# Optimization experiments

Measured on AMD Instinct MI355X. Metric: run time of the kernel, lower is better.

## Reference

```python
import jax, jax.numpy as jnp
import numpy as np

NUM_BLOCKS = 2
RES_LAYERS = 10
RC, DC, SC, EC, OC, GC = 32, 32, 1024, 512, 256, 5
RF = NUM_BLOCKS * (2 ** RES_LAYERS - 1)  # receptive/residual field = 2046


def _conv(x, w, dil, pad_left):
    # x: (N, C, L), w: (O, I, K). Causal: left pad only (equivalent to
    # torch padding=d followed by slicing off the last d samples).
    return jax.lax.conv_general_dilated(
        x, w, window_strides=(1,), padding=[(pad_left, 0)],
        rhs_dilation=(dil,), dimension_numbers=('NCH', 'OIH', 'NCH'))


def setup_inputs() -> dict:
    key = jax.random.key(0)
    ks = jax.random.split(key, 13)
    B, L = 2, 8192
    nl = NUM_BLOCKS * RES_LAYERS
    s = lambda k, shape, sc: (jax.random.normal(k, shape, jnp.float32) * sc)
    return {
        'inputs': s(ks[0], (B, 256, L), 1.0),
        'conditioning': s(ks[1], (B, GC), 1.0),
        'input_w': s(ks[2], (RC, 256, 1), 0.06),
        'filter_w': s(ks[3], (nl, DC, RC, 2), 0.12),
        'gate_w': s(ks[4], (nl, DC, RC, 2), 0.12),
        'res_w': s(ks[5], (nl, RC, DC, 1), 0.17),
        'split_w': s(ks[6], (nl, SC, DC, 1), 0.17),
        'gcf_w': s(ks[7], (nl, 1, GC), 0.3),
        'gcs_w': s(ks[8], (nl, 1, GC), 0.3),
        'f1_w': s(ks[9], (EC, SC, 1), 0.03),
        'f1_b': jnp.zeros((EC,), jnp.float32),
        'f2_w': s(ks[10], (OC, EC, 1), 0.04),
        'f2_b': jnp.zeros((OC,), jnp.float32),
    }


def reference(inputs, conditioning, input_w, filter_w, gate_w, res_w,
              split_w, gcf_w, gcs_w, f1_w, f1_b, f2_w, f2_b):
    L = inputs.shape[2]
    tgt = L - RF  # target_length
    res = _conv(inputs, input_w, 1, 0)  # (B, RC, L)
    final = jnp.zeros((inputs.shape[0], SC, tgt), inputs.dtype)
    for b in range(NUM_BLOCKS):
        for l in range(RES_LAYERS):
            i = b * RES_LAYERS + l
            d = 2 ** l
            f = _conv(res, filter_w[i], d, d)  # causal dilated, length L
            g = _conv(res, gate_w[i], d, d)
            # global conditioning: Linear(GC,1) -> per-batch scalar, broadcast
            gc_f = (conditioning @ gcf_w[i].T)[:, None, :]  # (B,1,1)
            gc_g = (conditioning @ gcs_w[i].T)[:, None, :]
            out = jnp.tanh(f + gc_f) * jax.nn.sigmoid(g + gc_g)
            res = _conv(out, res_w[i], 1, 0) + res
            final = final + _conv(out, split_w[i], 1, 0)[:, :, -tgt:]
    x = jax.nn.relu(final)
    x = _conv(x, f1_w, 1, 0) + f1_b[None, :, None]
    x = jax.nn.relu(x)
    x = _conv(x, f2_w, 1, 0) + f2_b[None, :, None]
    n, c, ln = x.shape
    return jnp.transpose(x, (0, 2, 1)).reshape(n * ln, c)
```

## Files before the change

### kernel.cpp

```cpp
#include <hip/hip_runtime.h>
#include <hip/hip_bf16.h>
#include <cstddef>

#define Bc   2
#define Lc   8192
#define TGT  6146
#define NL   20
#define RCc  32
#define DCc  32
#define SCc  1024
#define ECc  512
#define OCc  256
#define KTOT (NL * DCc)
#define TTILES 49
#define T64   97

typedef __attribute__((ext_vector_type(4))) float f32x4;
typedef __attribute__((ext_vector_type(8))) short bf16x8;
typedef __attribute__((ext_vector_type(4))) int i32x4;
typedef __attribute__((ext_vector_type(2))) int i32x2;

typedef __attribute__((address_space(1))) void* as1v;
typedef __attribute__((address_space(3))) void* as3v;

__device__ inline bf16x8 cvt8(const float4* p) {
    float4 a = p[0], b = p[1];
    union { bf16x8 v; __hip_bfloat16 h[8]; } u;
    u.h[0] = __float2bfloat16(a.x); u.h[1] = __float2bfloat16(a.y);
    u.h[2] = __float2bfloat16(a.z); u.h[3] = __float2bfloat16(a.w);
    u.h[4] = __float2bfloat16(b.x); u.h[5] = __float2bfloat16(b.y);
    u.h[6] = __float2bfloat16(b.z); u.h[7] = __float2bfloat16(b.w);
    return u.v;
}

__global__ __launch_bounds__(256) void prep_kernel(
    const float* __restrict__ x,
    const float* __restrict__ iw,
    float* __restrict__ res_out,
    const float* __restrict__ split_w,
    const float* __restrict__ f1_w,
    const float* __restrict__ f2_w,
    const float* __restrict__ filt,
    const float* __restrict__ gate,
    const float* __restrict__ resw,
    __hip_bfloat16* __restrict__ Wp1,
    __hip_bfloat16* __restrict__ Wp2,
    __hip_bfloat16* __restrict__ Wp3,
    __hip_bfloat16* __restrict__ wfgp,
    __hip_bfloat16* __restrict__ wrp,
    int npack)
{
    __shared__ float ws[32][256];
    __shared__ float xs[64][64];
    int tid = threadIdx.x;

    if ((int)blockIdx.x < npack) {
        int idx = blockIdx.x * 256 + tid;
        const int N1 = SCc * KTOT, N2 = ECc * SCc, N3 = OCc * ECc, N4 = NL * 64 * 64;
        if (idx < N1) {
            int m = idx / KTOT, k = idx % KTOT;
            int i = k >> 5, c = k & 31;
            Wp1[idx] = __float2bfloat16(split_w[((size_t)i * SCc + m) * DCc + c]);
            return;
        }
        idx -= N1;
        if (idx < N2) { Wp2[idx] = __float2bfloat16(f1_w[idx]); return; }
        idx -= N2;
        if (idx < N3) { Wp3[idx] = __float2bfloat16(f2_w[idx]); return; }
        idx -= N3;
        if (idx < N4) {
            int li = idx / 4096, r = idx % 4096;
            int m = r >> 6, k = r & 63;
            int tap = k >> 5, ic = k & 31;
            float v = (m < 32) ? filt[(size_t)li * 2048 + (m * 32 + ic) * 2 + tap]
                               : gate[(size_t)li * 2048 + ((m - 32) * 32 + ic) * 2 + tap];
            int slot = (k >> 3) ^ (m & 7);
            wfgp[((size_t)li * 64 + m) * 64 + slot * 8 + (k & 7)] = __float2bfloat16(v);
            if (r < 2048) {
                int m2 = r >> 6;
                float v2 = (k < 32) ? resw[(size_t)li * 1024 + m2 * 32 + k] : 0.f;
                wrp[((size_t)li * 32 + m2) * 64 + slot * 8 + (k & 7)] = __float2bfloat16(v2);
            }
        }
        return;
    }

    int bid = blockIdx.x - npack;
    int b   = bid >> 7;
    int t0  = (bid & 127) * 64;

    for (int idx = tid; idx < 32 * 256; idx += 256)
        ws[idx >> 8][idx & 255] = iw[idx];

    int tl = tid & 63, qq = tid >> 6, oc0 = qq * 8;
    float acc[8] = {};

    for (int icc = 0; icc < 4; ++icc) {
        __syncthreads();
        for (int idx = tid; idx < 64 * 64; idx += 256) {
            int icl = idx >> 6, tll = idx & 63;
            xs[icl][tll] = x[((size_t)b * 256 + icc * 64 + icl) * Lc + t0 + tll];
        }
        __syncthreads();
        for (int icl = 0; icl < 64; icl += 4) {
            float x0 = xs[icl][tl], x1 = xs[icl + 1][tl];
            float x2 = xs[icl + 2][tl], x3 = xs[icl + 3][tl];
#pragma unroll
            for (int j = 0; j < 8; ++j) {
                const float4 w4 = *(const float4*)&ws[oc0 + j][icc * 64 + icl];
                acc[j] += w4.x * x0 + w4.y * x1 + w4.z * x2 + w4.w * x3;
            }
        }
    }
#pragma unroll
    for (int j = 0; j < 8; ++j)
        res_out[((size_t)b * 32 + oc0 + j) * Lc + t0 + tl] = acc[j];
}

__global__ __launch_bounds__(512) void layer_group5(
    const float* __restrict__ res_in,
    float* __restrict__ res_out,
    __hip_bfloat16* __restrict__ outsT,
    const __hip_bfloat16* __restrict__ wfgp,
    const __hip_bfloat16* __restrict__ wrp,
    const float* __restrict__ cond,
    const float* __restrict__ gcf_w,
    const float* __restrict__ gcs_w,
    int l0)
{
    constexpr int W = 96, H = 32, NT = 6;
    __shared__ __align__(16) float resL[W * 36];
    __shared__ __align__(16) unsigned short OsL[W * 40];
    __shared__ __align__(16) i32x4 Wf[2][64 * 8];
    __shared__ __align__(16) i32x4 Wrs[2][32 * 8];

    int tid  = threadIdx.x;
    int b    = blockIdx.y;
    int t0   = blockIdx.x * 64;
    int lane = tid & 63, wid = tid >> 6;
    int r15  = lane & 15, q = lane >> 4;

    const float* rb = res_in + (size_t)b * 32 * Lc;
    for (int idx = tid; idx < W * 32; idx += 512) {
        int ch = idx / W, tl = idx % W;
        int tg = t0 - H + tl;
        resL[tl * 36 + ch] = (tg >= 0) ? rb[(size_t)ch * Lc + tg] : 0.f;
    }

    auto issueW = [&](int bufi, int li2) {
        const __hip_bfloat16* wfg = wfgp + (size_t)li2 * 4096;
        const __hip_bfloat16* wrl = wrp  + (size_t)li2 * 2048;
        __builtin_amdgcn_global_load_lds(
            (as1v)(void*)((const i32x4*)wfg + wid * 64 + lane),
            (as3v)(void*)&Wf[bufi][wid * 64], 16, 0, 0);
        if (wid < 4)
            __builtin_amdgcn_global_load_lds(
                (as1v)(void*)((const i32x4*)wrl + wid * 64 + lane),
                (as3v)(void*)&Wrs[bufi][wid * 64], 16, 0, 0);
    };
    issueW(0, l0);

#pragma unroll
    for (int i = 0; i < 5; ++i) {
        const int cur = i & 1;
        int li = l0 + i;
        int d  = 1 << i;

        float gf = 0.f, gg = 0.f;
#pragma unroll
        for (int c = 0; c < 5; ++c) {
            gf += gcf_w[li * 5 + c] * cond[b * 5 + c];
            gg += gcs_w[li * 5 + c] * cond[b * 5 + c];
        }
        __syncthreads();
        if (i + 1 < 5) issueW(cur ^ 1, li + 1);

        const bf16x8* Wv = (const bf16x8*)Wf[cur];
        for (int tt = wid; tt < NT; tt += 8) {
            int ct0 = tt * 16;
            int srow0 = ct0 + r15 - d; if (srow0 < 0) srow0 = 0;
            int srow1 = ct0 + r15;
            bf16x8 a0 = cvt8((const float4*)&resL[srow0 * 36 + q * 8]);
            bf16x8 a1 = cvt8((const float4*)&resL[srow1 * 36 + q * 8]);
            int sg0 = q ^ (r15 & 7), sg1 = (4 + q) ^ (r15 & 7);
            f32x4 acc[4] = {};
#pragma unroll
            for (int fj = 0; fj < 4; ++fj)
                acc[fj] = __builtin_amdgcn_mfma_f32_16x16x32_bf16(
                    a0, Wv[(fj * 16 + r15) * 8 + sg0], acc[fj], 0, 0, 0);
#pragma unroll
            for (int fj = 0; fj < 4; ++fj)
                acc[fj] = __builtin_amdgcn_mfma_f32_16x16x32_bf16(
                    a1, Wv[(fj * 16 + r15) * 8 + sg1], acc[fj], 0, 0, 0);
#pragma unroll
            for (int fj = 0; fj < 2; ++fj) {
#pragma unroll
                for (int r = 0; r < 4; ++r) {
                    float F = acc[fj][r] + gf;
                    float G = acc[fj + 2][r] + gg;
                    float th  = 1.f - 2.f / (__expf(2.f * F) + 1.f);
                    float sgm = 1.f / (1.f + __expf(-G));
                    float o   = th * sgm;
                    int col = ct0 + q * 4 + r;
                    int ch  = fj * 16 + r15;
                    __hip_bfloat16 ob = __float2bfloat16(o);
                    OsL[col * 40 + ch] = *(unsigned short*)&ob;
                }
            }
        }
        __syncthreads();

        {
            int row = tid >> 3, chunk = tid & 7;
            int tg = t0 + row;
            if (tg >= Lc - TGT) {
                i32x2 v = *(const i32x2*)&OsL[(H + row) * 40 + chunk * 4];
                *(i32x2*)(outsT + ((size_t)(b * TGT + tg - (Lc - TGT))) * KTOT
                          + li * 32 + chunk * 4) = v;
            }
        }

        const bf16x8* Rv = (const bf16x8*)Wrs[cur];
        const bf16x8* Ov = (const bf16x8*)OsL;
        for (int tt = wid; tt < NT; tt += 8) {
            int ct0 = tt * 16;
            bf16x8 ao = Ov[(ct0 + r15) * 5 + q];
            int sg = q ^ (r15 & 7);
            f32x4 racc[2] = {};
#pragma unroll
            for (int fj = 0; fj < 2; ++fj)
                racc[fj] = __builtin_amdgcn_mfma_f32_16x16x32_bf16(
                    ao, Rv[(fj * 16 + r15) * 8 + sg], racc[fj], 0, 0, 0);
#pragma unroll
            for (int fj = 0; fj < 2; ++fj)
#pragma unroll
                for (int r = 0; r < 4; ++r) {
                    int col = ct0 + q * 4 + r;
                    int ch  = fj * 16 + r15;
                    if (t0 + col - H >= 0)
                        resL[col * 36 + ch] += racc[fj][r];
                }
        }
    }
    __syncthreads();

    {
        int ch = tid >> 4, t4 = (tid & 15) * 4;
        float v[4];
#pragma unroll
        for (int j = 0; j < 4; ++j) v[j] = resL[(H + t4 + j) * 36 + ch];
        float* ro = res_out + ((size_t)(b * 32) + ch) * Lc + t0 + t4;
        *(float4*)ro = make_float4(v[0], v[1], v[2], v[3]);
    }
}

template <bool LASTHALF>
__global__ __launch_bounds__(512) void layer_groupS(
    const float* __restrict__ res_in,
    float* __restrict__ res_out,
    __hip_bfloat16* __restrict__ outsT,
    const __hip_bfloat16* __restrict__ wfgp,
    const __hip_bfloat16* __restrict__ wrp,
    const float* __restrict__ cond,
    const float* __restrict__ gcf_w,
    const float* __restrict__ gcs_w,
    int l0)
{
    constexpr int W = 96, H = 32, NT = 6, S = 32;
    __shared__ __align__(16) float resL[W * 36];
    __shared__ __align__(16) unsigned short OsL[W * 40];
    __shared__ __align__(16) i32x4 Wf[2][64 * 8];
    __shared__ __align__(16) i32x4 Wrs[2][32 * 8];

    int tid  = threadIdx.x;
    int b    = blockIdx.y;
    int r    = blockIdx.x & 31;
    int c0   = (blockIdx.x >> 5) * 64;
    int lane = tid & 63, wid = tid >> 6;
    int r15  = lane & 15, q = lane >> 4;

    const float* rb = res_in + (size_t)b * 32 * Lc;
    for (int idx = tid; idx < W * 32; idx += 512) {
        int ch = idx / W, col = idx % W;
        int cj = c0 + col - H;
        resL[col * 36 + ch] = (cj >= 0) ? rb[(size_t)ch * Lc + r + S * cj] : 0.f;
    }

    auto issueW = [&](int bufi, int li2) {
        const __hip_bfloat16* wfg = wfgp + (size_t)li2 * 4096;
        const __hip_bfloat16* wrl = wrp  + (size_t)li2 * 2048;
        __builtin_amdgcn_global_load_lds(
            (as1v)(void*)((const i32x4*)wfg + wid * 64 + lane),
            (as3v)(void*)&Wf[bufi][wid * 64], 16, 0, 0);
        if (wid < 4)
            __builtin_amdgcn_global_load_lds(
                (as1v)(void*)((const i32x4*)wrl + wid * 64 + lane),
                (as3v)(void*)&Wrs[bufi][wid * 64], 16, 0, 0);
    };
    issueW(0, l0);

#pragma unroll
    for (int i = 0; i < 5; ++i) {
        const int cur = i & 1;
        int li = l0 + i;
        int dc = 1 << i;

        float gf = 0.f, gg = 0.f;
#pragma unroll
        for (int c = 0; c < 5; ++c) {
            gf += gcf_w[li * 5 + c] * cond[b * 5 + c];
            gg += gcs_w[li * 5 + c] * cond[b * 5 + c];
        }
        __syncthreads();
        if (i + 1 < 5) issueW(cur ^ 1, li + 1);

        const bf16x8* Wv = (const bf16x8*)Wf[cur];
        for (int tt = wid; tt < NT; tt += 8) {
            int ct0 = tt * 16;
            int srow0 = ct0 + r15 - dc; if (srow0 < 0) srow0 = 0;
            int srow1 = ct0 + r15;
            bf16x8 a0 = cvt8((const float4*)&resL[srow0 * 36 + q * 8]);
            bf16x8 a1 = cvt8((const float4*)&resL[srow1 * 36 + q * 8]);
            int sg0 = q ^ (r15 & 7), sg1 = (4 + q) ^ (r15 & 7);
            f32x4 acc[4] = {};
#pragma unroll
            for (int fj = 0; fj < 4; ++fj)
                acc[fj] = __builtin_amdgcn_mfma_f32_16x16x32_bf16(
                    a0, Wv[(fj * 16 + r15) * 8 + sg0], acc[fj], 0, 0, 0);
#pragma unroll
            for (int fj = 0; fj < 4; ++fj)
                acc[fj] = __builtin_amdgcn_mfma_f32_16x16x32_bf16(
                    a1, Wv[(fj * 16 + r15) * 8 + sg1], acc[fj], 0, 0, 0);
#pragma unroll
            for (int fj = 0; fj < 2; ++fj) {
#pragma unroll
                for (int rr = 0; rr < 4; ++rr) {
                    float F = acc[fj][rr] + gf;
                    float G = acc[fj + 2][rr] + gg;
                    float th  = 1.f - 2.f / (__expf(2.f * F) + 1.f);
                    float sgm = 1.f / (1.f + __expf(-G));
                    float o   = th * sgm;
                    int col = ct0 + q * 4 + rr;
                    int ch  = fj * 16 + r15;
                    __hip_bfloat16 ob = __float2bfloat16(o);
                    OsL[col * 40 + ch] = *(unsigned short*)&ob;
                }
            }
        }
        __syncthreads();

        {
            int row = tid >> 3, chunk = tid & 7;
            int t = r + S * (c0 + row);
            if (t >= Lc - TGT) {
                i32x2 v = *(const i32x2*)&OsL[(H + row) * 40 + chunk * 4];
                *(i32x2*)(outsT + ((size_t)(b * TGT + t - (Lc - TGT))) * KTOT
                          + li * 32 + chunk * 4) = v;
            }
        }

        if (!(LASTHALF && i == 4)) {
            const bf16x8* Rv = (const bf16x8*)Wrs[cur];
            const bf16x8* Ov = (const bf16x8*)OsL;
            for (int tt = wid; tt < NT; tt += 8) {
                int ct0 = tt * 16;
                bf16x8 ao = Ov[(ct0 + r15) * 5 + q];
                int sg = q ^ (r15 & 7);
                f32x4 racc[2] = {};
#pragma unroll
                for (int fj = 0; fj < 2; ++fj)
                    racc[fj] = __builtin_amdgcn_mfma_f32_16x16x32_bf16(
                        ao, Rv[(fj * 16 + r15) * 8 + sg], racc[fj], 0, 0, 0);
#pragma unroll
                for (int fj = 0; fj < 2; ++fj)
#pragma unroll
                    for (int rr = 0; rr < 4; ++rr) {
                        int col = ct0 + q * 4 + rr;
                        int ch  = fj * 16 + r15;
                        if (c0 + col - H >= 0)
                            resL[col * 36 + ch] += racc[fj][rr];
                    }
            }
        }
    }

    if (!LASTHALF) {
        __syncthreads();
        int ch = tid >> 4, t4 = (tid & 15) * 4;
#pragma unroll
        for (int j = 0; j < 4; ++j) {
            int t = r + S * (c0 + t4 + j);
            res_out[((size_t)(b * 32) + ch) * Lc + t] = resL[(H + t4 + j) * 36 + ch];
        }
    }
}

template <bool RELU_OUT, int NKT>
__global__ __launch_bounds__(256) void gemm_mfma64(
    const __hip_bfloat16* __restrict__ X,
    const __hip_bfloat16* __restrict__ W,
    const float* __restrict__ bias,
    __hip_bfloat16* __restrict__ Y,
    int M, int MB)
{
    constexpr int K = NKT * 64;
    __shared__ __align__(16) char smem[49152];
    i32x4* Xs0 = (i32x4*)smem;
    i32x4* Ws0 = (i32x4*)(smem + 16384);
    i32x4* Xs1 = (i32x4*)(smem + 24576);
    i32x4* Ws1 = (i32x4*)(smem + 40960);

    int nwg  = gridDim.x;
    int orig = blockIdx.x;
    int q8 = nwg >> 3, r8 = nwg & 7;
    int xcd = orig & 7, loc = orig >> 3;
    int wgid = (xcd < r8 ? xcd * (q8 + 1) : r8 * (q8 + 1) + (xcd - r8) * q8) + loc;
    int mi  = wgid % MB;
    int byy = wgid / MB;
    int b   = byy / TTILES;
    int t0  = (byy % TTILES) * 128;
    int m0  = mi * 64;

    int tid = threadIdx.x;
    int lane = tid & 63, wid = tid >> 6;
    int r15 = lane & 15, q = lane >> 4;

    int subrow = lane >> 3;
    int g      = (lane & 7) ^ subrow;
    const __hip_bfloat16* xp[4];
    const __hip_bfloat16* wp[2];
#pragma unroll
    for (int i = 0; i < 4; ++i) {
        int r = wid * 32 + i * 8 + subrow;
        int xrow = t0 + r; if (xrow > TGT - 1) xrow = TGT - 1;
        xp[i] = X + ((size_t)(b * TGT + xrow)) * K + g * 8;
    }
#pragma unroll
    for (int i = 0; i < 2; ++i) {
        int r = wid * 16 + i * 8 + subrow;
        wp[i] = W + ((size_t)(m0 + r)) * K + g * 8;
    }

    f32x4 acc[2][4] = {};

#define STAGE(XB, WB)                                                          \
    {                                                                          \
        _Pragma("unroll")                                                      \
        for (int i = 0; i < 4; ++i) {                                          \
            __builtin_amdgcn_global_load_lds((as1v)(void*)xp[i],               \
                (as3v)(void*)&XB[(wid * 4 + i) * 64], 16, 0, 0);               \
            xp[i] += 64;                                                       \
        }                                                                      \
        _Pragma("unroll")                                                      \
        for (int i = 0; i < 2; ++i) {                                          \
            __builtin_amdgcn_global_load_lds((as1v)(void*)wp[i],               \
                (as3v)(void*)&WB[(wid * 2 + i) * 64], 16, 0, 0);               \
            wp[i] += 64;                                                       \
        }                                                                      \
    }

    auto compute = [&](const i32x4* Xb, const i32x4* Wb) {
        const bf16x8* Xv = (const bf16x8*)Xb;
        const bf16x8* Wv = (const bf16x8*)Wb;
#pragma unroll
        for (int kk = 0; kk < 2; ++kk) {
            int sg = (kk * 4 + q) ^ (r15 & 7);
            bf16x8 af[2], bw[4];
#pragma unroll
            for (int ft = 0; ft < 2; ++ft)
                af[ft] = Xv[(wid * 32 + ft * 16 + r15) * 8 + sg];
#pragma unroll
            for (int fj = 0; fj < 4; ++fj)
                bw[fj] = Wv[(fj * 16 + r15) * 8 + sg];
#pragma unroll
            for (int ft = 0; ft < 2; ++ft)
#pragma unroll
                for (int fj = 0; fj < 4; ++fj)
                    acc[ft][fj] = __builtin_amdgcn_mfma_f32_16x16x32_bf16(
                        af[ft], bw[fj], acc[ft][fj], 0, 0, 0);
        }
    };

    STAGE(Xs0, Ws0);

#pragma unroll
    for (int kt2 = 0; kt2 < NKT; kt2 += 2) {
        STAGE(Xs1, Ws1);
        asm volatile("s_waitcnt vmcnt(6)" ::: "memory");
        __builtin_amdgcn_s_barrier();
        __builtin_amdgcn_sched_barrier(0);
        __builtin_amdgcn_s_setprio(1);
        compute(Xs0, Ws0);
        __builtin_amdgcn_s_setprio(0);
        __builtin_amdgcn_sched_barrier(0);
        __builtin_amdgcn_s_barrier();

        if (kt2 + 2 < NKT) {
            STAGE(Xs0, Ws0);
            asm volatile("s_waitcnt vmcnt(6)" ::: "memory");
        } else {
            asm volatile("s_waitcnt vmcnt(0)" ::: "memory");
        }
        __builtin_amdgcn_s_barrier();
        __builtin_amdgcn_sched_barrier(0);
        __builtin_amdgcn_s_setprio(1);
        compute(Xs1, Ws1);
        __builtin_amdgcn_s_setprio(0);
        __builtin_amdgcn_sched_barrier(0);
        __builtin_amdgcn_s_barrier();
    }
#undef STAGE

    __hip_bfloat16* Eb = (__hip_bfloat16*)smem;
#pragma unroll
    for (int ft = 0; ft < 2; ++ft) {
#pragma unroll
        for (int r = 0; r < 4; ++r) {
            int tl = wid * 32 + ft * 16 + q * 4 + r;
#pragma unroll
            for (int fj = 0; fj < 4; ++fj) {
                int ml = fj * 16 + r15;
                float v = acc[ft][fj][r];
                if (bias) v += bias[m0 + ml];
                if (RELU_OUT) v = fmaxf(v, 0.f);
                Eb[tl * 72 + ml] = __float2bfloat16(v);
            }
        }
    }
    __syncthreads();
    {
        int row = tid >> 1, half = tid & 1;
        int t = t0 + row;
        if (t < TGT) {
            __hip_bfloat16* dst = Y + ((size_t)(b * TGT + t)) * M + m0 + half * 32;
            const __hip_bfloat16* src = Eb + row * 72 + half * 32;
#pragma unroll
            for (int k = 0; k < 4; ++k)
                ((i32x4*)dst)[k] = ((const i32x4*)src)[k];
        }
    }
}

__global__ __launch_bounds__(512) void gemm_fused23(
    const __hip_bfloat16* __restrict__ X,
    const __hip_bfloat16* __restrict__ W2,
    const float* __restrict__ b1,
    const __hip_bfloat16* __restrict__ W3,
    const float* __restrict__ b2,
    float* __restrict__ Y)
{
    __shared__ __align__(16) char smem[153600];
    i32x4* Xs[2] = { (i32x4*)smem, (i32x4*)(smem + 8192) };
    i32x4* Ws[2] = { (i32x4*)(smem + 16384), (i32x4*)(smem + 81920) };
    __hip_bfloat16* Hs = (__hip_bfloat16*)(smem + 16384);
    i32x4* W3s[2] = { (i32x4*)(smem + 88064), (i32x4*)(smem + 120832) };

    int nwg  = gridDim.x;
    int orig = blockIdx.x;
    int q8 = nwg >> 3, r8 = nwg & 7;
    int xcd = orig & 7, loc = orig >> 3;
    int wgid = (xcd < r8 ? xcd * (q8 + 1) : r8 * (q8 + 1) + (xcd - r8) * q8) + loc;
    int b  = wgid / T64;
    int t0 = (wgid % T64) * 64;

    int tid = threadIdx.x;
    int lane = tid & 63, wid = tid >> 6;
    int r15 = lane & 15, q = lane >> 4;
    int subrow = lane >> 3;
    int g      = (lane & 7) ^ subrow;

    int xr = wid * 8 + subrow;
    int xrow = t0 + xr; if (xrow > TGT - 1) xrow = TGT - 1;
    const __hip_bfloat16* xp = X + ((size_t)(b * TGT + xrow)) * SCc + g * 8;
    const __hip_bfloat16* wp[8];
#pragma unroll
    for (int i = 0; i < 8; ++i)
        wp[i] = W2 + ((size_t)((wid * 8 + i) * 8 + subrow)) * SCc + g * 8;

    f32x4 acc[4][4] = {};

#define STAGEA(bi)                                                             \
    {                                                                          \
        __builtin_amdgcn_global_load_lds((as1v)(void*)xp,                      \
            (as3v)(void*)&Xs[bi][wid * 64], 16, 0, 0);                         \
        xp += 64;                                                              \
        _Pragma("unroll")                                                      \
        for (int i = 0; i < 8; ++i) {                                          \
            __builtin_amdgcn_global_load_lds((as1v)(void*)wp[i],               \
                (as3v)(void*)&Ws[bi][(wid * 8 + i) * 64], 16, 0, 0);           \
            wp[i] += 64;                                                       \
        }                                                                      \
    }

    auto computeA = [&](const i32x4* Xb, const i32x4* Wb) {
        const bf16x8* Xv = (const bf16x8*)Xb;
        const bf16x8* Wv = (const bf16x8*)Wb;
#pragma unroll
        for (int kk = 0; kk < 2; ++kk) {
            int sg = (kk * 4 + q) ^ (r15 & 7);
            bf16x8 af[4], bw[4];
#pragma unroll
            for (int ft = 0; ft < 4; ++ft)
                af[ft] = Xv[(ft * 16 + r15) * 8 + sg];
#pragma unroll
            for (int fj = 0; fj < 4; ++fj)
                bw[fj] = Wv[(wid * 64 + fj * 16 + r15) * 8 + sg];
#pragma unroll
            for (int ft = 0; ft < 4; ++ft)
#pragma unroll
                for (int fj = 0; fj < 4; ++fj)
                    acc[ft][fj] = __builtin_amdgcn_mfma_f32_16x16x32_bf16(
                        af[ft], bw[fj], acc[ft][fj], 0, 0, 0);
        }
    };

    STAGEA(0);
#pragma unroll
    for (int kt = 0; kt < 16; ++kt) {
        const int cur = kt & 1;
        if (kt + 1 < 16) {
            STAGEA(cur ^ 1);
            asm volatile("s_waitcnt vmcnt(9)" ::: "memory");
        } else {
            asm volatile("s_waitcnt vmcnt(0)" ::: "memory");
        }
        __builtin_amdgcn_s_barrier();
        __builtin_amdgcn_sched_barrier(0);
        __builtin_amdgcn_s_setprio(1);
        computeA(Xs[cur], Ws[cur]);
        __builtin_amdgcn_s_setprio(0);
        __builtin_amdgcn_sched_barrier(0);
        __builtin_amdgcn_s_barrier();
    }
#undef STAGEA

#pragma unroll
    for (int ft = 0; ft < 4; ++ft) {
#pragma unroll
        for (int r = 0; r < 4; ++r) {
            int tl = ft * 16 + q * 4 + r;
#pragma unroll
            for (int fj = 0; fj < 4; ++fj) {
                int m = wid * 64 + fj * 16 + r15;
                float v = acc[ft][fj][r] + b1[m];
                v = fmaxf(v, 0.f);
                Hs[tl * 520 + m] = __float2bfloat16(v);
            }
        }
    }

    const __hip_bfloat16* w3p[4];
#pragma unroll
    for (int i = 0; i < 4; ++i)
        w3p[i] = W3 + ((size_t)((wid * 4 + i) * 8 + subrow)) * ECc + g * 8;

#define STAGEB(bi)                                                             \
    {                                                                          \
        _Pragma("unroll")                                                      \
        for (int i = 0; i < 4; ++i) {                                          \
            __builtin_amdgcn_global_load_lds((as1v)(void*)w3p[i],              \
                (as3v)(void*)&W3s[bi][(wid * 4 + i) * 64], 16, 0, 0);          \
            w3p[i] += 64;                                                      \
        }                                                                      \
    }

    STAGEB(0);
    __syncthreads();

    f32x4 accB[4][2] = {};

#pragma unroll
    for (int kt = 0; kt < 8; ++kt) {
        const int cur = kt & 1;
        if (kt + 1 < 8) {
            STAGEB(cur ^ 1);
            asm volatile("s_waitcnt vmcnt(4)" ::: "memory");
        } else {
            asm volatile("s_waitcnt vmcnt(0)" ::: "memory");
        }
        __builtin_amdgcn_s_barrier();
        __builtin_amdgcn_sched_barrier(0);
        __builtin_amdgcn_s_setprio(1);
        {
            const bf16x8* Wv = (const bf16x8*)W3s[cur];
#pragma unroll
            for (int kk = 0; kk < 2; ++kk) {
                int gk = kt * 8 + kk * 4 + q;
                int sg = (kk * 4 + q) ^ (r15 & 7);
                bf16x8 af[4], bw[2];
#pragma unroll
                for (int ft = 0; ft < 4; ++ft)
                    af[ft] = *(const bf16x8*)&Hs[(ft * 16 + r15) * 520 + gk * 8];
#pragma unroll
                for (int fj = 0; fj < 2; ++fj)
                    bw[fj] = Wv[(wid * 32 + fj * 16 + r15) * 8 + sg];
#pragma unroll
                for (int ft = 0; ft < 4; ++ft)
#pragma unroll
                    for (int fj = 0; fj < 2; ++fj)
                        accB[ft][fj] = __builtin_amdgcn_mfma_f32_16x16x32_bf16(
                            af[ft], bw[fj], accB[ft][fj], 0, 0, 0);
            }
        }
        __builtin_amdgcn_s_setprio(0);
        __builtin_amdgcn_sched_barrier(0);
        __builtin_amdgcn_s_barrier();
    }
#undef STAGEB

#pragma unroll
    for (int ft = 0; ft < 4; ++ft) {
#pragma unroll
        for (int r = 0; r < 4; ++r) {
            int t = t0 + ft * 16 + q * 4 + r;
            if (t < TGT) {
                size_t rowoff = ((size_t)(b * TGT + t)) * OCc;
#pragma unroll
                for (int fj = 0; fj < 2; ++fj) {
                    int m = wid * 32 + fj * 16 + r15;
                    Y[rowoff + m] = accB[ft][fj][r] + b2[m];
                }
            }
        }
    }
}

extern "C" void kernel_launch(void* const* d_in, const int* in_sizes, int n_in,
                              void* d_out, int out_size, void* d_ws, size_t ws_size,
                              hipStream_t stream)
{
    const float* inputs   = (const float*)d_in[0];
    const float* cond     = (const float*)d_in[1];
    const float* input_w  = (const float*)d_in[2];
    const float* filter_w = (const float*)d_in[3];
    const float* gate_w   = (const float*)d_in[4];
    const float* res_w    = (const float*)d_in[5];
    const float* split_w  = (const float*)d_in[6];
    const float* gcf_w    = (const float*)d_in[7];
    const float* gcs_w    = (const float*)d_in[8];
    const float* f1_w     = (const float*)d_in[9];
    const float* f1_b     = (const float*)d_in[10];
    const float* f2_w     = (const float*)d_in[11];
    const float* f2_b     = (const float*)d_in[12];
    float* out = (float*)d_out;

    char* wsb = (char*)d_ws;
    const size_t RES_B   = (size_t)Bc * RCc * Lc * 4;
    const size_t OUTS_B  = (size_t)Bc * TGT * KTOT * 2;
    const size_t FIN_B   = (size_t)Bc * TGT * SCc * 2;
    const size_t W1_B    = (size_t)SCc * KTOT * 2;
    const size_t W2_B    = (size_t)ECc * SCc * 2;
    const size_t W3_B    = (size_t)OCc * ECc * 2;
    const size_t WFG_B   = (size_t)NL * 64 * 64 * 2;
    const size_t WR_B    = (size_t)NL * 32 * 64 * 2;

    float* res0              = (float*)wsb;                   size_t off = RES_B;
    float* res1              = (float*)(wsb + off);           off += RES_B;
    __hip_bfloat16* outsT    = (__hip_bfloat16*)(wsb + off);  off += OUTS_B;
    __hip_bfloat16* finalT   = (__hip_bfloat16*)(wsb + off);  off += FIN_B;
    __hip_bfloat16* Wp1      = (__hip_bfloat16*)(wsb + off);  off += W1_B;
    __hip_bfloat16* Wp2      = (__hip_bfloat16*)(wsb + off);  off += W2_B;
    __hip_bfloat16* Wp3      = (__hip_bfloat16*)(wsb + off);  off += W3_B;
    __hip_bfloat16* wfgp     = (__hip_bfloat16*)(wsb + off);  off += WFG_B;
    __hip_bfloat16* wrp      = (__hip_bfloat16*)(wsb + off);  off += WR_B;

    {
        const int NTOT = SCc * KTOT + ECc * SCc + OCc * ECc + NL * 64 * 64;
        const int npack = (NTOT + 255) / 256;
        prep_kernel<<<npack + Bc * 128, 256, 0, stream>>>(
            inputs, input_w, res0,
            split_w, f1_w, f2_w, filter_w, gate_w, res_w,
            Wp1, Wp2, Wp3, wfgp, wrp, npack);
    }

    float* rin = res0;
    float* rout = res1;
    const dim3 lgrid(Lc / 64, Bc);
    const dim3 sgrid(128, Bc);

    layer_group5<<<lgrid, 512, 0, stream>>>(
        rin, rout, outsT, wfgp, wrp, cond, gcf_w, gcs_w, 0);
    { float* t = rin; rin = rout; rout = t; }
    layer_groupS<false><<<sgrid, 512, 0, stream>>>(
        rin, rout, outsT, wfgp, wrp, cond, gcf_w, gcs_w, 5);
    { float* t = rin; rin = rout; rout = t; }
    layer_group5<<<lgrid, 512, 0, stream>>>(
        rin, rout, outsT, wfgp, wrp, cond, gcf_w, gcs_w, 10);
    { float* t = rin; rin = rout; rout = t; }
    layer_groupS<true><<<sgrid, 512, 0, stream>>>(
        rin, rout, outsT, wfgp, wrp, cond, gcf_w, gcs_w, 15);

    gemm_mfma64<true, 10><<<(SCc / 64) * Bc * TTILES, 256, 0, stream>>>(
        outsT, Wp1, nullptr, finalT, SCc, SCc / 64);

    gemm_fused23<<<Bc * T64, 512, 0, stream>>>(
        finalT, Wp2, f1_b, Wp3, f2_b, out);
}
```

Before: 163.1 us.

## Double-buffer residual tile in LDS, drop mid-layer barrier, skip unneeded early tiles

The residual tile in LDS is split into two ping-pong buffers (resA/resB). Each wave now owns one 16-column tile and does the gated activation, the outsT store and the residual MFMA update without the barrier that used to sit between them, leaving one __syncthreads per layer. The third layer-group launch also starts at tile 15 and skips early time tiles. Causality means those tiles cannot reach the target window or later layers. The cost is more LDS per block, which may lower occupancy, and a reliance on intra-wave ordering of LDS writes and reads.

Measured after the change: 156.3 us, median of 3. 1.04x faster.

```diff
diff --git a/kernel.cpp b/kernel.cpp
--- a/kernel.cpp
+++ b/kernel.cpp
@@ -126,17 +126,18 @@
     const float* __restrict__ cond,
     const float* __restrict__ gcf_w,
     const float* __restrict__ gcs_w,
-    int l0)
+    int l0, int t0off)
 {
     constexpr int W = 96, H = 32, NT = 6;
-    __shared__ __align__(16) float resL[W * 36];
+    __shared__ __align__(16) float resA[W * 36];
+    __shared__ __align__(16) float resB[W * 36];
     __shared__ __align__(16) unsigned short OsL[W * 40];
     __shared__ __align__(16) i32x4 Wf[2][64 * 8];
     __shared__ __align__(16) i32x4 Wrs[2][32 * 8];
 
     int tid  = threadIdx.x;
     int b    = blockIdx.y;
-    int t0   = blockIdx.x * 64;
+    int t0   = (t0off + blockIdx.x) * 64;
     int lane = tid & 63, wid = tid >> 6;
     int r15  = lane & 15, q = lane >> 4;
 
@@ -144,7 +145,7 @@
     for (int idx = tid; idx < W * 32; idx += 512) {
         int ch = idx / W, tl = idx % W;
         int tg = t0 - H + tl;
-        resL[tl * 36 + ch] = (tg >= 0) ? rb[(size_t)ch * Lc + tg] : 0.f;
+        resA[tl * 36 + ch] = (tg >= 0) ? rb[(size_t)ch * Lc + tg] : 0.f;
     }
 
     auto issueW = [&](int bufi, int li2) {
@@ -163,6 +164,8 @@
 #pragma unroll
     for (int i = 0; i < 5; ++i) {
         const int cur = i & 1;
+        const float* rc = cur ? resB : resA;
+        float*       rn = cur ? resA : resB;
         int li = l0 + i;
         int d  = 1 << i;
 
@@ -175,13 +178,13 @@
         __syncthreads();
         if (i + 1 < 5) issueW(cur ^ 1, li + 1);
 
-        const bf16x8* Wv = (const bf16x8*)Wf[cur];
-        for (int tt = wid; tt < NT; tt += 8) {
-            int ct0 = tt * 16;
+        if (wid < NT) {
+            int ct0 = wid * 16;
+            const bf16x8* Wv = (const bf16x8*)Wf[cur];
             int srow0 = ct0 + r15 - d; if (srow0 < 0) srow0 = 0;
             int srow1 = ct0 + r15;
-            bf16x8 a0 = cvt8((const float4*)&resL[srow0 * 36 + q * 8]);
-            bf16x8 a1 = cvt8((const float4*)&resL[srow1 * 36 + q * 8]);
+            bf16x8 a0 = cvt8((const float4*)&rc[srow0 * 36 + q * 8]);
+            bf16x8 a1 = cvt8((const float4*)&rc[srow1 * 36 + q * 8]);
             int sg0 = q ^ (r15 & 7), sg1 = (4 + q) ^ (r15 & 7);
             f32x4 acc[4] = {};
 #pragma unroll
@@ -207,23 +210,20 @@
                     OsL[col * 40 + ch] = *(unsigned short*)&ob;
                 }
             }
-        }
-        __syncthreads();
-
-        {
-            int row = tid >> 3, chunk = tid & 7;
-            int tg = t0 + row;
-            if (tg >= Lc - TGT) {
-                i32x2 v = *(const i32x2*)&OsL[(H + row) * 40 + chunk * 4];
-                *(i32x2*)(outsT + ((size_t)(b * TGT + tg - (Lc - TGT))) * KTOT
-                          + li * 32 + chunk * 4) = v;
-            }
-        }
-
-        const bf16x8* Rv = (const bf16x8*)Wrs[cur];
-        const bf16x8* Ov = (const bf16x8*)OsL;
-        for (int tt = wid; tt < NT; tt += 8) {
-            int ct0 = tt * 16;
+
+            {
+                int col = ct0 + (lane >> 2), chunk = lane & 3;
+                if (col >= H) {
+                    int t = t0 + col - H;
+                    if (t >= Lc - TGT)
+                        *(i32x4*)(outsT + ((size_t)(b * TGT + t - (Lc - TGT))) * KTOT
+                                  + li * 32 + chunk * 8) =
+                            *(const i32x4*)&OsL[col * 40 + chunk * 8];
+                }
+            }
+
+            const bf16x8* Rv = (const bf16x8*)Wrs[cur];
+            const bf16x8* Ov = (const bf16x8*)OsL;
             bf16x8 ao = Ov[(ct0 + r15) * 5 + q];
             int sg = q ^ (r15 & 7);
             f32x4 racc[2] = {};
@@ -237,8 +237,8 @@
                 for (int r = 0; r < 4; ++r) {
                     int col = ct0 + q * 4 + r;
                     int ch  = fj * 16 + r15;
-                    if (t0 + col - H >= 0)
-                        resL[col * 36 + ch] += racc[fj][r];
+                    float base = rc[col * 36 + ch];
+                    rn[col * 36 + ch] = (t0 + col - H >= 0) ? base + racc[fj][r] : base;
                 }
         }
     }
@@ -248,7 +248,7 @@
         int ch = tid >> 4, t4 = (tid & 15) * 4;
         float v[4];
 #pragma unroll
-        for (int j = 0; j < 4; ++j) v[j] = resL[(H + t4 + j) * 36 + ch];
+        for (int j = 0; j < 4; ++j) v[j] = resB[(H + t4 + j) * 36 + ch];
         float* ro = res_out + ((size_t)(b * 32) + ch) * Lc + t0 + t4;
         *(float4*)ro = make_float4(v[0], v[1], v[2], v[3]);
     }
@@ -267,7 +267,8 @@
     int l0)
 {
     constexpr int W = 96, H = 32, NT = 6, S = 32;
-    __shared__ __align__(16) float resL[W * 36];
+    __shared__ __align__(16) float resA[W * 36];
+    __shared__ __align__(16) float resB[W * 36];
     __shared__ __align__(16) unsigned short OsL[W * 40];
     __shared__ __align__(16) i32x4 Wf[2][64 * 8];
     __shared__ __align__(16) i32x4 Wrs[2][32 * 8];
@@ -283,7 +284,7 @@
     for (int idx = tid; idx < W * 32; idx += 512) {
         int ch = idx / W, col = idx % W;
         int cj = c0 + col - H;
-        resL[col * 36 + ch] = (cj >= 0) ? rb[(size_t)ch * Lc + r + S * cj] : 0.f;
+        resA[col * 36 + ch] = (cj >= 0) ? rb[(size_t)ch * Lc + r + S * cj] : 0.f;
     }
 
     auto issueW = [&](int bufi, int li2) {
@@ -302,6 +303,8 @@
 #pragma unroll
     for (int i = 0; i < 5; ++i) {
         const int cur = i & 1;
+        const float* rc = cur ? resB : resA;
+        float*       rn = cur ? resA : resB;
         int li = l0 + i;
         int dc = 1 << i;
 
@@ -314,13 +317,13 @@
         __syncthreads();
         if (i + 1 < 5) issueW(cur ^ 1, li + 1);
 
-        const bf16x8* Wv = (const bf16x8*)Wf[cur];
-        for (int tt = wid; tt < NT; tt += 8) {
-            int ct0 = tt * 16;
+        if (wid < NT) {
+            int ct0 = wid * 16;
+            const bf16x8* Wv = (const bf16x8*)Wf[cur];
             int srow0 = ct0 + r15 - dc; if (srow0 < 0) srow0 = 0;
             int srow1 = ct0 + r15;
-            bf16x8 a0 = cvt8((const float4*)&resL[srow0 * 36 + q * 8]);
-            bf16x8 a1 = cvt8((const float4*)&resL[srow1 * 36 + q * 8]);
+            bf16x8 a0 = cvt8((const float4*)&rc[srow0 * 36 + q * 8]);
+            bf16x8 a1 = cvt8((const float4*)&rc[srow1 * 36 + q * 8]);
             int sg0 = q ^ (r15 & 7), sg1 = (4 + q) ^ (r15 & 7);
             f32x4 acc[4] = {};
 #pragma unroll
@@ -346,24 +349,21 @@
                     OsL[col * 40 + ch] = *(unsigned short*)&ob;
                 }
             }
-        }
-        __syncthreads();
-
-        {
-            int row = tid >> 3, chunk = tid & 7;
-            int t = r + S * (c0 + row);
-            if (t >= Lc - TGT) {
-                i32x2 v = *(const i32x2*)&OsL[(H + row) * 40 + chunk * 4];
-                *(i32x2*)(outsT + ((size_t)(b * TGT + t - (Lc - TGT))) * KTOT
-                          + li * 32 + chunk * 4) = v;
-            }
-        }
-
-        if (!(LASTHALF && i == 4)) {
-            const bf16x8* Rv = (const bf16x8*)Wrs[cur];
-            const bf16x8* Ov = (const bf16x8*)OsL;
-            for (int tt = wid; tt < NT; tt += 8) {
-                int ct0 = tt * 16;
+
+            {
+                int col = ct0 + (lane >> 2), chunk = lane & 3;
+                if (col >= H) {
+                    int t = r + S * (c0 + col - H);
+                    if (t >= Lc - TGT)
+                        *(i32x4*)(outsT + ((size_t)(b * TGT + t - (Lc - TGT))) * KTOT
+                                  + li * 32 + chunk * 8) =
+                            *(const i32x4*)&OsL[col * 40 + chunk * 8];
+                }
+            }
+
+            if (!(LASTHALF && i == 4)) {
+                const bf16x8* Rv = (const bf16x8*)Wrs[cur];
+                const bf16x8* Ov = (const bf16x8*)OsL;
                 bf16x8 ao = Ov[(ct0 + r15) * 5 + q];
                 int sg = q ^ (r15 & 7);
                 f32x4 racc[2] = {};
@@ -377,8 +377,8 @@
                     for (int rr = 0; rr < 4; ++rr) {
                         int col = ct0 + q * 4 + rr;
                         int ch  = fj * 16 + r15;
-                        if (c0 + col - H >= 0)
-                            resL[col * 36 + ch] += racc[fj][rr];
+                        float base = rc[col * 36 + ch];
+                        rn[col * 36 + ch] = (c0 + col - H >= 0) ? base + racc[fj][rr] : base;
                     }
             }
         }
@@ -390,7 +390,7 @@
 #pragma unroll
         for (int j = 0; j < 4; ++j) {
             int t = r + S * (c0 + t4 + j);
-            res_out[((size_t)(b * 32) + ch) * Lc + t] = resL[(H + t4 + j) * 36 + ch];
+            res_out[((size_t)(b * 32) + ch) * Lc + t] = resB[(H + t4 + j) * 36 + ch];
         }
     }
 }
@@ -775,17 +775,16 @@
 
     float* rin = res0;
     float* rout = res1;
-    const dim3 lgrid(Lc / 64, Bc);
     const dim3 sgrid(128, Bc);
 
-    layer_group5<<<lgrid, 512, 0, stream>>>(
-        rin, rout, outsT, wfgp, wrp, cond, gcf_w, gcs_w, 0);
+    layer_group5<<<dim3(128, Bc), 512, 0, stream>>>(
+        rin, rout, outsT, wfgp, wrp, cond, gcf_w, gcs_w, 0, 0);
     { float* t = rin; rin = rout; rout = t; }
     layer_groupS<false><<<sgrid, 512, 0, stream>>>(
         rin, rout, outsT, wfgp, wrp, cond, gcf_w, gcs_w, 5);
     { float* t = rin; rin = rout; rout = t; }
-    layer_group5<<<lgrid, 512, 0, stream>>>(
-        rin, rout, outsT, wfgp, wrp, cond, gcf_w, gcs_w, 10);
+    layer_group5<<<dim3(113, Bc), 512, 0, stream>>>(
+        rin, rout, outsT, wfgp, wrp, cond, gcf_w, gcs_w, 10, 15);
     { float* t = rin; rin = rout; rout = t; }
     layer_groupS<true><<<sgrid, 512, 0, stream>>>(
         rin, rout, outsT, wfgp, wrp, cond, gcf_w, gcs_w, 15);
```
